# Kernel tuning notes

Hardware: AMD Instinct MI355X
Metric: run time of the kernel (lower is better)

Reference implementation:

```python
import jax, jax.numpy as jnp
import numpy as np

B, H, W, DIM = 1, 320, 320, 256
WIN, NH = 10, 8
HD = DIM // NH
N = WIN * WIN
HID = 4 * DIM
SCALE = HD ** (-0.5)
EPS = 1e-5


def _rel_pos_index():
    coords = np.stack(np.meshgrid(np.arange(WIN), np.arange(WIN), indexing='ij'))  # [2,w,w]
    cf = coords.reshape(2, -1)                      # [2, N]
    rel = (cf[:, :, None] - cf[:, None, :]).transpose(1, 2, 0).astype(np.int64)  # [N,N,2]
    rel[:, :, 0] += WIN - 1
    rel[:, :, 1] += WIN - 1
    rel[:, :, 0] *= 2 * WIN - 1
    return jnp.asarray(rel.sum(-1))                 # [N, N]

REL_IDX = _rel_pos_index()


def setup_inputs() -> dict:
    key = jax.random.key(0)
    ks = jax.random.split(key, 16)
    std = 0.02
    return {
        'x': jax.random.normal(ks[0], (B, H * W, DIM), jnp.float32),
        'norm1_g': jnp.ones((DIM,), jnp.float32),
        'norm1_b': jnp.zeros((DIM,), jnp.float32),
        'wq': jax.random.normal(ks[1], (DIM, DIM), jnp.float32) * std,
        'bq': jnp.zeros((DIM,), jnp.float32),
        'wkv': jax.random.normal(ks[2], (DIM, 2 * DIM), jnp.float32) * std,
        'bkv': jnp.zeros((2 * DIM,), jnp.float32),
        'rpb': jax.random.normal(ks[3], ((2 * WIN - 1) ** 2, NH), jnp.float32) * std,
        'proj_w': jax.random.normal(ks[4], (DIM, DIM), jnp.float32) * std,
        'proj_b': jnp.zeros((DIM,), jnp.float32),
        'norm2_g': jnp.ones((DIM,), jnp.float32),
        'norm2_b': jnp.zeros((DIM,), jnp.float32),
        'l1_w': jax.random.normal(ks[5], (DIM, HID), jnp.float32) * std,
        'l1_b': jnp.zeros((HID,), jnp.float32),
        'dw_w': jax.random.normal(ks[6], (HID, 1, 3, 3), jnp.float32) * std,
        'dw_b': jnp.zeros((HID,), jnp.float32),
        'l2_w': jax.random.normal(ks[7], (HID, DIM), jnp.float32) * std,
        'l2_b': jnp.zeros((DIM,), jnp.float32),
    }


def _ln(x, g, b):
    m = x.mean(-1, keepdims=True)
    v = ((x - m) ** 2).mean(-1, keepdims=True)
    return (x - m) * jax.lax.rsqrt(v + EPS) * g + b


def reference(x, norm1_g, norm1_b, wq, bq, wkv, bkv, rpb, proj_w, proj_b,
              norm2_g, norm2_b, l1_w, l1_b, dw_w, dw_b, l2_w, l2_b):
    # ---- Window attention branch ----
    h = _ln(x, norm1_g, norm1_b).reshape(B, H, W, DIM)
    # window partition: [B*nW, N, C]
    win = h.reshape(B, H // WIN, WIN, W // WIN, WIN, DIM)
    win = win.transpose(0, 1, 3, 2, 4, 5).reshape(-1, N, DIM)
    q = (win @ wq + bq).reshape(-1, N, NH, HD).transpose(0, 2, 1, 3) * SCALE  # [bW,h,N,d]
    kv = (win @ wkv + bkv).reshape(-1, N, 2, NH, HD).transpose(2, 0, 3, 1, 4)
    k, v = kv[0], kv[1]                                                        # [bW,h,N,d]
    attn = jnp.einsum('bhnd,bhmd->bhnm', q, k)                                 # [bW,h,N,N]
    bias = rpb[REL_IDX]                                                        # [N,N,h]
    attn = attn + bias.transpose(2, 0, 1)[None]
    attn = jax.nn.softmax(attn, axis=-1)
    o = jnp.einsum('bhnm,bhmd->bhnd', attn, v).transpose(0, 2, 1, 3).reshape(-1, N, DIM)
    o = o @ proj_w + proj_b
    # window reverse: [B, H*W, C]
    o = o.reshape(B, H // WIN, W // WIN, WIN, WIN, DIM)
    o = o.transpose(0, 1, 3, 2, 4, 5).reshape(B, H * W, DIM)
    x = x + o
    # ---- LeFF branch ----
    h2 = _ln(x, norm2_g, norm2_b)
    f = jax.nn.gelu(h2 @ l1_w + l1_b, approximate=False)
    f = f.reshape(B, H, W, HID).transpose(0, 3, 1, 2)                          # NCHW
    f = jax.lax.conv_general_dilated(
        f, dw_w, window_strides=(1, 1), padding='SAME',
        feature_group_count=HID,
        dimension_numbers=('NCHW', 'OIHW', 'NCHW')) + dw_b[None, :, None, None]
    f = jax.nn.gelu(f, approximate=False)
    f = f.transpose(0, 2, 3, 1).reshape(B, H * W, HID)
    x = x + (f @ l2_w + l2_b)
    return x
```

## Files before the change

### kernel.cpp

```cpp
#include <hip/hip_runtime.h>
#include <hip/hip_bf16.h>

typedef unsigned short u16;
typedef __attribute__((ext_vector_type(8))) __bf16 bf16x8;
typedef __attribute__((ext_vector_type(4))) float f32x4;

#define HW_ 320
#define DIM_ 256
#define HID_ 1024
#define SCALE_ 0.1767766952966369f
#define LDP 72
#define NEGINF_ -30000.0f

__device__ __forceinline__ float b2f(u16 u){
  union{unsigned int i; float f;} z; z.i=((unsigned int)u)<<16; return z.f;
}
__device__ __forceinline__ u16 f2b(float f){
  union{float f; unsigned int i;} z; z.f=f;
  return (u16)((z.i + 0x7fffu + ((z.i>>16)&1u))>>16);
}
__device__ __forceinline__ u16 f2b_s(float f, float sub){
  union{float f; unsigned int i;} z; z.f=f;
  if ((z.i & 0x7F800000u) == 0x7F800000u) z.f = sub;
  return (u16)((z.i + 0x7fffu + ((z.i>>16)&1u))>>16);
}
__device__ __forceinline__ float gelu_f(float v){
  float u = 0.7978845608028654f*(v + 0.044715f*v*v*v);
  float e = __expf(2.f*u);
  float t = 1.f - 2.f/(e+1.f);
  return 0.5f*v*(1.f+t);
}

__global__ void k_transpose(const float* __restrict__ src, u16* __restrict__ dst, int K, int N){
  int i = blockIdx.x*256 + threadIdx.x;
  if (i < K*N){ int k = i / N, n = i - k*N; dst[(size_t)n*K + k] = f2b(src[i]); }
}
__global__ void k_transpose_dw(const float* __restrict__ src, u16* __restrict__ dst){
  int i = blockIdx.x*256 + threadIdx.x;
  if (i < 9216){ int ch = i / 9, kk = i - ch*9; dst[kk*1024 + ch] = f2b(src[i]); }
}
__global__ void k_qkvbias(const float* __restrict__ bq, const float* __restrict__ bkv, float* __restrict__ dst){
  int i = blockIdx.x*256 + threadIdx.x;
  if (i < 768) dst[i] = (i<256) ? bq[i] : bkv[i-256];
}
__global__ void k_biastab(const float* __restrict__ rpb, float* __restrict__ btab){
  int i = blockIdx.x*256 + threadIdx.x;
  if (i >= 114688) return;
  int ct = i & 7, lr = (i>>3) & 15;
  int idx = i >> 7;
  int n = idx % 112, h = idx / 112;
  int m = ct*16 + lr;
  float v = NEGINF_;
  if (n < 100 && m < 100){
    int rel = (n/10 - m/10 + 9)*19 + (n%10 - m%10 + 9);
    v = rpb[rel*8 + h];
  }
  btab[i] = v;
}

template<int F32IN, int WINDOWED>
__global__ __launch_bounds__(256) void k_ln(const void* __restrict__ xv,
    const float* __restrict__ g, const float* __restrict__ b, u16* __restrict__ out)
{
  int tid = threadIdx.x, lane = tid & 63;
  int t = blockIdx.x*4 + (tid>>6);
  float v[4];
  if constexpr (F32IN){
    float4 f = *(const float4*)((const float*)xv + (size_t)t*DIM_ + lane*4);
    v[0]=f.x; v[1]=f.y; v[2]=f.z; v[3]=f.w;
  } else {
    uint2 u = *(const uint2*)((const u16*)xv + (size_t)t*DIM_ + lane*4);
    v[0]=b2f((u16)(u.x&0xffff)); v[1]=b2f((u16)(u.x>>16));
    v[2]=b2f((u16)(u.y&0xffff)); v[3]=b2f((u16)(u.y>>16));
  }
  float s  = v[0]+v[1]+v[2]+v[3];
  float ss = v[0]*v[0]+v[1]*v[1]+v[2]*v[2]+v[3]*v[3];
  for (int m=1;m<64;m<<=1){ s += __shfl_xor(s,m,64); ss += __shfl_xor(ss,m,64); }
  float mean = s*(1.0f/DIM_);
  float var  = ss*(1.0f/DIM_) - mean*mean;
  if (var < 0.f) var = 0.f;
  float rstd = rsqrtf(var + 1e-5f);
  float4 gg = *(const float4*)(g + lane*4);
  float4 bb = *(const float4*)(b + lane*4);
  float o0 = (v[0]-mean)*rstd*gg.x + bb.x;
  float o1 = (v[1]-mean)*rstd*gg.y + bb.y;
  float o2 = (v[2]-mean)*rstd*gg.z + bb.z;
  float o3 = (v[3]-mean)*rstd*gg.w + bb.w;
  int row = t;
  if constexpr (WINDOWED){
    int hy = t / HW_, wx = t - hy*HW_;
    row = ((hy/10)*32 + wx/10)*100 + (hy%10)*10 + (wx%10);
  }
  unsigned lo = (unsigned)f2b(o0) | ((unsigned)f2b(o1)<<16);
  unsigned hi = (unsigned)f2b(o2) | ((unsigned)f2b(o3)<<16);
  *(uint2*)(out + (size_t)row*DIM_ + lane*4) = make_uint2(lo,hi);
}

template<int EPI, int CLAMP>
__global__ __launch_bounds__(256) void k_gemm(
    const u16* __restrict__ A, const u16* __restrict__ Bt, int K, int nx,
    const float* __restrict__ biasf,
    const float* __restrict__ resf, const u16* __restrict__ resb,
    u16* __restrict__ O0, u16* __restrict__ O1, u16* __restrict__ O2,
    float* __restrict__ Of,
    int a_off, int o_off)
{
  __shared__ u16 Al[128*LDP];
  __shared__ u16 Bl[128*LDP];
  int tid = threadIdx.x;
  int bid = blockIdx.x, nwg = gridDim.x;
  int swz = (bid & 7)*(nwg>>3) + (bid>>3);
  int m0 = (swz / nx)*128, n0 = (swz % nx)*128;
  int w = tid>>6, lane = tid&63, lr = lane&15, lg = lane>>4;
  int wrow = (w>>1)*64, wcol = (w&1)*64;
  f32x4 zero = {0.f,0.f,0.f,0.f};
  f32x4 acc[4][4];
  #pragma unroll
  for (int i=0;i<4;++i)
    #pragma unroll
    for (int j=0;j<4;++j) acc[i][j]=zero;

  for (int kt=0; kt<K; kt+=64){
    #pragma unroll
    for (int it=0; it<4; ++it){
      int vi = tid + it*256;
      int row = vi>>3, cv = (vi&7)*8;
      *(bf16x8*)&Bl[row*LDP+cv] = *(const bf16x8*)(Bt + (size_t)(n0+row)*K + kt + cv);
      int srow = m0 + row;
      if constexpr (CLAMP){
        srow += a_off;
        srow = srow < 0 ? 0 : (srow > 102399 ? 102399 : srow);
      }
      *(bf16x8*)&Al[row*LDP+cv] = *(const bf16x8*)(A + (size_t)srow*K + kt + cv);
    }
    __syncthreads();
    #pragma unroll
    for (int k0=0;k0<64;k0+=32){
      bf16x8 af[4], bfr[4];
      #pragma unroll
      for (int i=0;i<4;++i) af[i]  = *(const bf16x8*)&Al[(wrow+i*16+lr)*LDP + k0 + lg*8];
      #pragma unroll
      for (int j=0;j<4;++j) bfr[j] = *(const bf16x8*)&Bl[(wcol+j*16+lr)*LDP + k0 + lg*8];
      #pragma unroll
      for (int i=0;i<4;++i)
        #pragma unroll
        for (int j=0;j<4;++j)
          acc[i][j] = __builtin_amdgcn_mfma_f32_16x16x32_bf16(af[i], bfr[j], acc[i][j],0,0,0);
    }
    __syncthreads();
  }

  #pragma unroll
  for (int i=0;i<4;++i){
    #pragma unroll
    for (int j=0;j<4;++j){
      #pragma unroll
      for (int r=0;r<4;++r){
        int grow = m0 + wrow + i*16 + lg*4 + r;
        int gcol = n0 + wcol + j*16 + lr;
        float v = acc[i][j][r];
        if constexpr (EPI==0){
          v += biasf[gcol];
          int winl = grow/100, n = grow - winl*100;
          int part = gcol>>8, c = gcol&255;
          size_t idx = ((size_t)(winl*8 + (c>>5))*100 + n)*32 + (c&31);
          if (part==0)      O0[idx] = f2b_s(v*SCALE_, 10000.f);
          else if (part==1) O1[idx] = f2b_s(v, 10000.f);
          else              O2[idx] = f2b_s(v, 10000.f);
        } else if constexpr (EPI==1){
          int win = grow/100, n = grow - win*100;
          int wy = win>>5, wxx = win&31;
          int py = n/10, px = n - py*10;
          size_t t = (size_t)((wy*10+py)*HW_ + wxx*10 + px);
          float o = v + biasf[gcol] + resf[t*DIM_ + gcol];
          O0[t*DIM_ + gcol] = f2b_s(o, 30000.f);
        } else if constexpr (EPI==2){
          float o = gelu_f(v + biasf[gcol]);
          O0[(size_t)grow*HID_ + gcol] = f2b_s(o, 40000.f);
        } else {
          size_t t = (size_t)(o_off + grow);
          float o = v + biasf[gcol] + b2f(resb[t*DIM_ + gcol]);
          union{float f; unsigned int i;} z; z.f=o;
          if ((z.i & 0x7F800000u) == 0x7F800000u) o = 60000.f;
          Of[t*DIM_ + gcol] = o;
        }
      }
    }
  }
}

__global__ __launch_bounds__(256) void k_attn(
    const u16* __restrict__ Q, const u16* __restrict__ Kb, const u16* __restrict__ Vb,
    const float* __restrict__ btab, u16* __restrict__ Ow)
{
  __shared__ u16 p_lds[112*136];
  __shared__ u16 v_t[32*136];
  int tid = threadIdx.x;
  int wh = blockIdx.x;
  int head = wh & 7, win = wh >> 3;
  for (int i=tid;i<896;i+=256){ int row=i>>3, c=i&7; *(unsigned*)&p_lds[row*136 + 112 + 2*c] = 0u; }
  for (int i=tid;i<576;i+=256){ int d=i/18, c=i-18*d; *(unsigned*)&v_t[d*136 + 100 + 2*c] = 0u; }
  __syncthreads();
  const u16* vbase = Vb + (size_t)wh*3200;
  for (int i=tid;i<1600;i+=256){
    int m=i>>4, d2=(i&15)<<1;
    unsigned u = *(const unsigned*)(vbase + m*32 + d2);
    v_t[d2*136+m]     = (u16)(u&0xffff);
    v_t[(d2+1)*136+m] = (u16)(u>>16);
  }

  int w = tid>>6, lane = tid&63, lr = lane&15, lg = lane>>4;
  const u16* qbase = Q  + (size_t)wh*3200;
  const u16* kbase = Kb + (size_t)wh*3200;
  f32x4 zero = {0.f,0.f,0.f,0.f};
  bf16x8 aq[2];
  #pragma unroll
  for (int rt=0;rt<2;++rt){
    int qr = w*32 + rt*16 + lr; if (qr>99) qr=99;
    aq[rt] = *(const bf16x8*)(qbase + qr*32 + lg*8);
  }
  f32x4 s[2][7];
  #pragma unroll
  for (int ct=0;ct<7;++ct){
    int kr = ct*16 + lr; if (kr>99) kr=99;
    bf16x8 bk = *(const bf16x8*)(kbase + kr*32 + lg*8);
    s[0][ct] = __builtin_amdgcn_mfma_f32_16x16x32_bf16(aq[0], bk, zero,0,0,0);
    s[1][ct] = __builtin_amdgcn_mfma_f32_16x16x32_bf16(aq[1], bk, zero,0,0,0);
  }
  float inv[2][4];
  #pragma unroll
  for (int rt=0;rt<2;++rt){
    #pragma unroll
    for (int r=0;r<4;++r){
      int n = w*32 + rt*16 + lg*4 + r;
      int nb = n < 112 ? n : 111;
      const float* brow = btab + (((size_t)(head*112 + nb))*16 + lr)*8;
      float4 b0 = *(const float4*)brow;
      float4 b1 = *(const float4*)(brow + 4);
      float bias7[7] = {b0.x,b0.y,b0.z,b0.w,b1.x,b1.y,b1.z};
      float sm = 0.f;
      #pragma unroll
      for (int ct=0;ct<7;++ct){
        float p = __expf(s[rt][ct][r] + bias7[ct]);
        s[rt][ct][r] = p; sm += p;
      }
      #pragma unroll
      for (int msk=1;msk<16;msk<<=1) sm += __shfl_xor(sm,msk,64);
      inv[rt][r] = 1.f/sm;
      if (n < 112){
        #pragma unroll
        for (int ct=0;ct<7;++ct) p_lds[n*136 + ct*16 + lr] = f2b(s[rt][ct][r]);
      }
    }
  }
  __syncthreads();
  f32x4 o[2][2];
  o[0][0]=zero; o[0][1]=zero; o[1][0]=zero; o[1][1]=zero;
  #pragma unroll
  for (int k0=0;k0<128;k0+=32){
    bf16x8 ap[2];
    #pragma unroll
    for (int rt=0;rt<2;++rt){
      int pr = w*32 + rt*16 + lr; if (pr>111) pr=111;
      ap[rt] = *(const bf16x8*)&p_lds[pr*136 + k0 + lg*8];
    }
    #pragma unroll
    for (int dt=0;dt<2;++dt){
      bf16x8 bv = *(const bf16x8*)&v_t[(dt*16+lr)*136 + k0 + lg*8];
      o[0][dt] = __builtin_amdgcn_mfma_f32_16x16x32_bf16(ap[0], bv, o[0][dt],0,0,0);
      o[1][dt] = __builtin_amdgcn_mfma_f32_16x16x32_bf16(ap[1], bv, o[1][dt],0,0,0);
    }
  }
  #pragma unroll
  for (int rt=0;rt<2;++rt){
    #pragma unroll
    for (int dt=0;dt<2;++dt){
      #pragma unroll
      for (int r=0;r<4;++r){
        int n = w*32 + rt*16 + lg*4 + r;
        if (n<100)
          Ow[((size_t)(win*100+n))*DIM_ + head*32 + dt*16 + lr] = f2b_s(o[rt][dt][r]*inv[rt][r], 20000.f);
      }
    }
  }
}

#define YT_ 10
__global__ __launch_bounds__(256) void k_dwconv2(const u16* __restrict__ f,
    const u16* __restrict__ wT, const float* __restrict__ bias,
    u16* __restrict__ g, int y0)
{
  int tid = threadIdx.x;
  int bid = blockIdx.x;
  int xt = bid % 160, yt = bid / 160;
  int x  = xt*2 + (tid>>7);
  int cg = (tid&127)<<3;
  int yl0 = yt*YT_;

  float w[9][8];
  #pragma unroll
  for (int kk=0;kk<9;++kk){
    uint4 u = *(const uint4*)(wT + kk*1024 + cg);
    const unsigned* up=(const unsigned*)&u;
    #pragma unroll
    for(int e=0;e<4;++e){ w[kk][2*e]=b2f((u16)(up[e]&0xffff)); w[kk][2*e+1]=b2f((u16)(up[e]>>16)); }
  }
  float bs[8];
  {
    float4 b0 = *(const float4*)(bias+cg);
    float4 b1 = *(const float4*)(bias+cg+4);
    bs[0]=b0.x;bs[1]=b0.y;bs[2]=b0.z;bs[3]=b0.w;bs[4]=b1.x;bs[5]=b1.y;bs[6]=b1.z;bs[7]=b1.w;
  }
  uint4 zq = make_uint4(0,0,0,0);
  auto ld = [&](int ytap, int xx)->uint4{
    int yy = y0 + ytap;
    if (xx<0 || xx>=HW_ || yy<0 || yy>=HW_) return zq;
    return *(const uint4*)(f + ((size_t)((ytap+1)*HW_+xx))*HID_ + cg);
  };
  uint4 a00=ld(yl0-1,x-1), a01=ld(yl0-1,x), a02=ld(yl0-1,x+1);
  uint4 a10=ld(yl0  ,x-1), a11=ld(yl0  ,x), a12=ld(yl0  ,x+1);
  #pragma unroll
  for (int r=0;r<YT_;++r){
    int yl = yl0 + r;
    uint4 a20=ld(yl+1,x-1), a21=ld(yl+1,x), a22=ld(yl+1,x+1);
    float acc[8];
    #pragma unroll
    for (int c=0;c<8;++c) acc[c]=bs[c];
    auto fma8 = [&](const uint4& a, const float (&wk)[8]){
      const unsigned* up=(const unsigned*)&a;
      #pragma unroll
      for(int e=0;e<4;++e){
        acc[2*e]   += b2f((u16)(up[e]&0xffff)) * wk[2*e];
        acc[2*e+1] += b2f((u16)(up[e]>>16))    * wk[2*e+1];
      }
    };
    fma8(a00,w[0]); fma8(a01,w[1]); fma8(a02,w[2]);
    fma8(a10,w[3]); fma8(a11,w[4]); fma8(a12,w[5]);
    fma8(a20,w[6]); fma8(a21,w[7]); fma8(a22,w[8]);
    u16 ov[8];
    #pragma unroll
    for (int c=0;c<8;++c) ov[c] = f2b_s(gelu_f(acc[c]), 50000.f);
    uint4 pack;
    pack.x = (unsigned)ov[0] | ((unsigned)ov[1]<<16);
    pack.y = (unsigned)ov[2] | ((unsigned)ov[3]<<16);
    pack.z = (unsigned)ov[4] | ((unsigned)ov[5]<<16);
    pack.w = (unsigned)ov[6] | ((unsigned)ov[7]<<16);
    *(uint4*)(g + ((size_t)(yl*HW_+x))*HID_ + cg) = pack;
    a00=a10;a01=a11;a02=a12; a10=a20;a11=a21;a12=a22;
  }
}

extern "C" void kernel_launch(void* const* d_in, const int* in_sizes, int n_in,
                              void* d_out, int out_size, void* d_ws, size_t ws_size,
                              hipStream_t stream)
{
  (void)in_sizes; (void)n_in; (void)out_size; (void)ws_size;
  const float* x     = (const float*)d_in[0];
  const float* n1g   = (const float*)d_in[1];
  const float* n1b   = (const float*)d_in[2];
  const float* wq    = (const float*)d_in[3];
  const float* bq    = (const float*)d_in[4];
  const float* wkv   = (const float*)d_in[5];
  const float* bkv   = (const float*)d_in[6];
  const float* rpb   = (const float*)d_in[7];
  const float* projw = (const float*)d_in[8];
  const float* projb = (const float*)d_in[9];
  const float* n2g   = (const float*)d_in[10];
  const float* n2b   = (const float*)d_in[11];
  const float* l1w   = (const float*)d_in[12];
  const float* l1b   = (const float*)d_in[13];
  const float* dww   = (const float*)d_in[14];
  const float* dwb   = (const float*)d_in[15];
  const float* l2w   = (const float*)d_in[16];
  const float* l2b   = (const float*)d_in[17];

  char* ws = (char*)d_ws;
  u16*   WqkvT   = (u16*)(ws + 0);
  u16*   projT   = (u16*)(ws + 393216);
  u16*   l1T     = (u16*)(ws + 524288);
  u16*   l2T     = (u16*)(ws + 1048576);
  float* qkvbias = (float*)(ws + 1572864);
  u16*   dwT     = (u16*)(ws + 1575936);
  float* btab    = (float*)(ws + 1594368);
  u16*   x1      = (u16*)(ws + 2097152);
  u16*   h2      = (u16*)(ws + 54525952);
  char*  BR      = ws + 106954752;
  u16* Qb    = (u16*)(BR + 0);
  u16* Kbuf  = (u16*)(BR + 52428800);
  u16* Vbuf  = (u16*)(BR + 104857600);
  u16* hwin  = (u16*)(ws + 264241152);
  u16* fband = (u16*)(BR + 0);
  u16* gband = (u16*)(BR + 106168320);
  u16* owin  = (u16*)d_out;
  float* outp = (float*)d_out;

  k_transpose<<<256, 256, 0, stream>>>(wq,   WqkvT,          256, 256);
  k_transpose<<<512, 256, 0, stream>>>(wkv,  WqkvT + 65536,  256, 512);
  k_transpose<<<256, 256, 0, stream>>>(projw, projT,         256, 256);
  k_transpose<<<1024,256, 0, stream>>>(l1w,  l1T,            256, 1024);
  k_transpose<<<1024,256, 0, stream>>>(l2w,  l2T,            1024, 256);
  k_transpose_dw<<<36, 256, 0, stream>>>(dww, dwT);
  k_qkvbias<<<3, 256, 0, stream>>>(bq, bkv, qkvbias);
  k_biastab<<<448, 256, 0, stream>>>(rpb, btab);

  k_ln<1,1><<<25600, 256, 0, stream>>>(x, n1g, n1b, hwin);
  k_gemm<0,0><<<4800, 256, 0, stream>>>(hwin, WqkvT, 256, 6,
      qkvbias, nullptr, nullptr, Qb, Kbuf, Vbuf, nullptr, 0, 0);
  k_attn<<<8192, 256, 0, stream>>>(Qb, Kbuf, Vbuf, btab, owin);
  k_gemm<1,0><<<1600, 256, 0, stream>>>(owin, projT, 256, 2,
      projb, x, nullptr, x1, nullptr, nullptr, nullptr, 0, 0);
  k_ln<0,0><<<25600, 256, 0, stream>>>(x1, n2g, n2b, h2);
  for (int b=0; b<2; ++b){
    int y0 = 160*b;
    k_gemm<2,1><<<3240, 256, 0, stream>>>(h2, l1T, 256, 8,
        l1b, nullptr, nullptr, fband, nullptr, nullptr, nullptr,
        (y0-1)*HW_, 0);
    k_dwconv2<<<2560, 256, 0, stream>>>(fband, dwT, dwb, gband, y0);
    k_gemm<3,0><<<800, 256, 0, stream>>>(gband, l2T, 1024, 2,
        l2b, nullptr, x1, nullptr, nullptr, nullptr, outp,
        0, y0*HW_);
  }
}
```

Baseline: 772.6 us.

## Enlarge GEMM tiles to 256x128 with 512-thread blocks and hoist bias loads

The GEMM kernel now uses 512-thread workgroups (8 waves) computing 256x128 output tiles, so each B tile in LDS is shared by twice as many rows and the grid is halved. The l1 GEMM gets a row guard because 51840 rows no longer divide evenly into 256-row tiles, and the gband buffer offset moves to make room for the padded fband output. The epilogue is restructured to load bias once per column and compute row indexing once per row. The larger LDS footprint and launch_bounds(512,2) may limit occupancy and register budget.

```diff
diff --git a/kernel.cpp b/kernel.cpp
--- a/kernel.cpp
+++ b/kernel.cpp
@@ -97,20 +97,20 @@
 }
 
 template<int EPI, int CLAMP>
-__global__ __launch_bounds__(256) void k_gemm(
+__global__ __launch_bounds__(512,2) void k_gemm(
     const u16* __restrict__ A, const u16* __restrict__ Bt, int K, int nx,
     const float* __restrict__ biasf,
     const float* __restrict__ resf, const u16* __restrict__ resb,
     u16* __restrict__ O0, u16* __restrict__ O1, u16* __restrict__ O2,
     float* __restrict__ Of,
-    int a_off, int o_off)
+    int a_off, int o_off, int mguard)
 {
-  __shared__ u16 Al[128*LDP];
+  __shared__ u16 Al[256*LDP];
   __shared__ u16 Bl[128*LDP];
   int tid = threadIdx.x;
   int bid = blockIdx.x, nwg = gridDim.x;
   int swz = (bid & 7)*(nwg>>3) + (bid>>3);
-  int m0 = (swz / nx)*128, n0 = (swz % nx)*128;
+  int m0 = (swz / nx)*256, n0 = (swz % nx)*128;
   int w = tid>>6, lane = tid&63, lr = lane&15, lg = lane>>4;
   int wrow = (w>>1)*64, wcol = (w&1)*64;
   f32x4 zero = {0.f,0.f,0.f,0.f};
@@ -123,9 +123,8 @@
   for (int kt=0; kt<K; kt+=64){
     #pragma unroll
     for (int it=0; it<4; ++it){
-      int vi = tid + it*256;
+      int vi = tid + it*512;
       int row = vi>>3, cv = (vi&7)*8;
-      *(bf16x8*)&Bl[row*LDP+cv] = *(const bf16x8*)(Bt + (size_t)(n0+row)*K + kt + cv);
       int srow = m0 + row;
       if constexpr (CLAMP){
         srow += a_off;
@@ -133,6 +132,12 @@
       }
       *(bf16x8*)&Al[row*LDP+cv] = *(const bf16x8*)(A + (size_t)srow*K + kt + cv);
     }
+    #pragma unroll
+    for (int it=0; it<2; ++it){
+      int vi = tid + it*512;
+      int row = vi>>3, cv = (vi&7)*8;
+      *(bf16x8*)&Bl[row*LDP+cv] = *(const bf16x8*)(Bt + (size_t)(n0+row)*K + kt + cv);
+    }
     __syncthreads();
     #pragma unroll
     for (int k0=0;k0<64;k0+=32){
@@ -150,36 +155,54 @@
     __syncthreads();
   }
 
+  float bj[4];
+  #pragma unroll
+  for (int j=0;j<4;++j) bj[j] = biasf[n0 + wcol + j*16 + lr];
+
   #pragma unroll
   for (int i=0;i<4;++i){
     #pragma unroll
-    for (int j=0;j<4;++j){
-      #pragma unroll
-      for (int r=0;r<4;++r){
-        int grow = m0 + wrow + i*16 + lg*4 + r;
-        int gcol = n0 + wcol + j*16 + lr;
-        float v = acc[i][j][r];
-        if constexpr (EPI==0){
-          v += biasf[gcol];
-          int winl = grow/100, n = grow - winl*100;
+    for (int r=0;r<4;++r){
+      int grow = m0 + wrow + i*16 + lg*4 + r;
+      if constexpr (EPI==0){
+        int winl = grow/100, n = grow - winl*100;
+        size_t rowb = ((size_t)winl*8)*3200 + (size_t)n*32;
+        #pragma unroll
+        for (int j=0;j<4;++j){
+          int gcol = n0 + wcol + j*16 + lr;
+          float v = acc[i][j][r] + bj[j];
           int part = gcol>>8, c = gcol&255;
-          size_t idx = ((size_t)(winl*8 + (c>>5))*100 + n)*32 + (c&31);
+          size_t idx = rowb + (size_t)(c>>5)*3200 + (c&31);
           if (part==0)      O0[idx] = f2b_s(v*SCALE_, 10000.f);
           else if (part==1) O1[idx] = f2b_s(v, 10000.f);
           else              O2[idx] = f2b_s(v, 10000.f);
-        } else if constexpr (EPI==1){
-          int win = grow/100, n = grow - win*100;
-          int wy = win>>5, wxx = win&31;
-          int py = n/10, px = n - py*10;
-          size_t t = (size_t)((wy*10+py)*HW_ + wxx*10 + px);
-          float o = v + biasf[gcol] + resf[t*DIM_ + gcol];
+        }
+      } else if constexpr (EPI==1){
+        int win = grow/100, n = grow - win*100;
+        int wy = win>>5, wxx = win&31;
+        int py = n/10, px = n - py*10;
+        size_t t = (size_t)((wy*10+py)*HW_ + wxx*10 + px);
+        #pragma unroll
+        for (int j=0;j<4;++j){
+          int gcol = n0 + wcol + j*16 + lr;
+          float o = acc[i][j][r] + bj[j] + resf[t*DIM_ + gcol];
           O0[t*DIM_ + gcol] = f2b_s(o, 30000.f);
-        } else if constexpr (EPI==2){
-          float o = gelu_f(v + biasf[gcol]);
-          O0[(size_t)grow*HID_ + gcol] = f2b_s(o, 40000.f);
-        } else {
-          size_t t = (size_t)(o_off + grow);
-          float o = v + biasf[gcol] + b2f(resb[t*DIM_ + gcol]);
+        }
+      } else if constexpr (EPI==2){
+        if (grow < mguard){
+          #pragma unroll
+          for (int j=0;j<4;++j){
+            int gcol = n0 + wcol + j*16 + lr;
+            float o = gelu_f(acc[i][j][r] + bj[j]);
+            O0[(size_t)grow*HID_ + gcol] = f2b_s(o, 40000.f);
+          }
+        }
+      } else {
+        size_t t = (size_t)(o_off + grow);
+        #pragma unroll
+        for (int j=0;j<4;++j){
+          int gcol = n0 + wcol + j*16 + lr;
+          float o = acc[i][j][r] + bj[j] + b2f(resb[t*DIM_ + gcol]);
           union{float f; unsigned int i;} z; z.f=o;
           if ((z.i & 0x7F800000u) == 0x7F800000u) o = 60000.f;
           Of[t*DIM_ + gcol] = o;
@@ -390,7 +413,7 @@
   u16* Vbuf  = (u16*)(BR + 104857600);
   u16* hwin  = (u16*)(ws + 264241152);
   u16* fband = (u16*)(BR + 0);
-  u16* gband = (u16*)(BR + 106168320);
+  u16* gband = (u16*)(BR + 106430464);
   u16* owin  = (u16*)d_out;
   float* outp = (float*)d_out;
 
@@ -404,20 +427,20 @@
   k_biastab<<<448, 256, 0, stream>>>(rpb, btab);
 
   k_ln<1,1><<<25600, 256, 0, stream>>>(x, n1g, n1b, hwin);
-  k_gemm<0,0><<<4800, 256, 0, stream>>>(hwin, WqkvT, 256, 6,
-      qkvbias, nullptr, nullptr, Qb, Kbuf, Vbuf, nullptr, 0, 0);
+  k_gemm<0,0><<<2400, 512, 0, stream>>>(hwin, WqkvT, 256, 6,
+      qkvbias, nullptr, nullptr, Qb, Kbuf, Vbuf, nullptr, 0, 0, 1<<30);
   k_attn<<<8192, 256, 0, stream>>>(Qb, Kbuf, Vbuf, btab, owin);
-  k_gemm<1,0><<<1600, 256, 0, stream>>>(owin, projT, 256, 2,
-      projb, x, nullptr, x1, nullptr, nullptr, nullptr, 0, 0);
+  k_gemm<1,0><<<800, 512, 0, stream>>>(owin, projT, 256, 2,
+      projb, x, nullptr, x1, nullptr, nullptr, nullptr, 0, 0, 1<<30);
   k_ln<0,0><<<25600, 256, 0, stream>>>(x1, n2g, n2b, h2);
   for (int b=0; b<2; ++b){
     int y0 = 160*b;
-    k_gemm<2,1><<<3240, 256, 0, stream>>>(h2, l1T, 256, 8,
+    k_gemm<2,1><<<1624, 512, 0, stream>>>(h2, l1T, 256, 8,
         l1b, nullptr, nullptr, fband, nullptr, nullptr, nullptr,
-        (y0-1)*HW_, 0);
+        (y0-1)*HW_, 0, 51840);
     k_dwconv2<<<2560, 256, 0, stream>>>(fband, dwT, dwb, gband, y0);
-    k_gemm<3,0><<<800, 256, 0, stream>>>(gband, l2T, 1024, 2,
+    k_gemm<3,0><<<400, 512, 0, stream>>>(gband, l2T, 1024, 2,
         l2b, nullptr, x1, nullptr, nullptr, nullptr, outp,
-        0, y0*HW_);
-  }
-}
+        0, y0*HW_, 1<<30);
+  }
+}
```

Result: slower. 789.4 us (+2.2%).
